# Performance work log

Measured on AMD Instinct MI355X. Metric: run time of the kernel, lower is better.

The kernel has to match this reference:

```python
import jax, jax.numpy as jnp
import numpy as np

HIDDEN = 1024
NUM_EXPERTS = 16
TOP_K = 6
EPS = 1e-10


def setup_inputs() -> dict:
    key = jax.random.key(0)
    k1, k2, k3, k4 = jax.random.split(key, 4)
    tokens = jax.random.normal(k1, (4, 2048, HIDDEN), dtype=jnp.float32)
    # torch.nn.Linear(hidden_size, num_experts): weight [E, H], bias [E]
    bound = 1.0 / np.sqrt(HIDDEN)
    router_w = jax.random.uniform(k2, (NUM_EXPERTS, HIDDEN), jnp.float32, -bound, bound)
    router_b = jax.random.uniform(k3, (NUM_EXPERTS,), jnp.float32, -bound, bound)
    # expert_weights = randn(E, H, H) / sqrt(H)
    expert_w = jax.random.normal(k4, (NUM_EXPERTS, HIDDEN, HIDDEN), dtype=jnp.float32) / np.sqrt(HIDDEN)
    return {"tokens": tokens, "router_w": router_w, "router_b": router_b, "expert_w": expert_w}


def reference(tokens, router_w, router_b, expert_w):
    B, S, H = tokens.shape
    E = expert_w.shape[0]
    T = B * S

    # Router: softmax -> top-k -> renormalize top-k probs
    logits = jnp.einsum("bsh,eh->bse", tokens, router_w) + router_b  # [B,S,E]
    probs = jax.nn.softmax(logits, axis=-1)
    top_p, top_i = jax.lax.top_k(probs, TOP_K)                        # [B,S,K]
    top_p = top_p / (jnp.sum(top_p, axis=-1, keepdims=True) + EPS)

    x = tokens.reshape(T, H)
    flat_i = top_i.reshape(T, TOP_K)
    flat_p = top_p.reshape(T, TOP_K)

    # Dense gate matrix [T, E]: scatter of normalized top-k weights.
    # Equivalent to the expand/sort/pad + weighted scatter-add restore.
    gate = jnp.zeros((T, E), dtype=flat_p.dtype)
    gate = gate.at[jnp.arange(T)[:, None], flat_i].add(flat_p)
    acc = jnp.maximum(jnp.sum(gate, axis=-1), EPS)  # weight accumulator (clamp min=1e-10)

    # Grouped GEMM equivalent: per-expert matmul weighted by gate, accumulated.
    out = jnp.zeros_like(x)
    for e in range(E):  # fixed, small structural loop over experts
        out = out + (x @ expert_w[e]) * gate[:, e:e + 1]
    out = (out / acc[:, None]).reshape(B, S, H)

    # 'dummy' gradient-connection term from restore_output_with_triton_and_gradients
    out = out + EPS * jnp.sum(top_p, axis=-1, keepdims=True)
    return out
```

## Files before the change

### kernel.cpp

```cpp
#include <hip/hip_runtime.h>
#include <cstdint>
#include <cstddef>

#define NE 16
#define TOPK 6
#define HID 1024
#define NTOK 8192
#define EPSF 1e-10f
#define CAP_ROWS 51200
#define MAXBLK 400

typedef short bf16x8 __attribute__((ext_vector_type(8)));
typedef float f32x4 __attribute__((ext_vector_type(4)));

__device__ __forceinline__ unsigned int f2bf_rne(float f) {
  union { float f; unsigned int u; } v;
  v.f = f;
  return (v.u + 0x7FFFu + ((v.u >> 16) & 1u)) >> 16;
}

__device__ __forceinline__ float bfbits2f(unsigned int hi16) {
  union { unsigned int u; float f; } v;
  v.u = hi16 << 16;
  return v.f;
}

__device__ __forceinline__ void load_lds16(const void* g, void* l) {
  __builtin_amdgcn_global_load_lds(
      (const __attribute__((address_space(1))) void*)g,
      (__attribute__((address_space(3))) void*)l, 16, 0, 0);
}

__global__ __launch_bounds__(256) void router_sparse_kernel(
    const float* __restrict__ tokens, const float* __restrict__ rw,
    const float* __restrict__ rb, unsigned short* __restrict__ Xb,
    unsigned int* __restrict__ topk, float* __restrict__ g6,
    float* __restrict__ epst) {
  __shared__ float s_rw[NE * HID];
  const int tid = threadIdx.x;
  const int wv = tid >> 6;
  const int lane = tid & 63;
  const int token = blockIdx.x * 4 + wv;

  for (int i = tid; i < NE * HID / 4; i += 256)
    ((float4*)s_rw)[i] = ((const float4*)rw)[i];
  __syncthreads();

  const float* xp = tokens + (size_t)token * HID;
  float x[16];
#pragma unroll
  for (int j = 0; j < 16; ++j) x[j] = xp[lane + 64 * j];

  unsigned short* xbrow = Xb + (size_t)token * HID;
#pragma unroll
  for (int j = 0; j < 16; ++j)
    xbrow[lane + 64 * j] = (unsigned short)f2bf_rne(x[j]);

  float lg[NE];
#pragma unroll
  for (int e = 0; e < NE; ++e) {
    const float* w = s_rw + e * HID;
    float p = 0.f;
#pragma unroll
    for (int j = 0; j < 16; ++j) p += x[j] * w[lane + 64 * j];
    lg[e] = p;
  }
#pragma unroll
  for (int m = 1; m < 64; m <<= 1) {
#pragma unroll
    for (int e = 0; e < NE; ++e) lg[e] += __shfl_xor(lg[e], m);
  }
  float mx = -1e30f;
#pragma unroll
  for (int e = 0; e < NE; ++e) {
    lg[e] += rb[e];
    mx = fmaxf(mx, lg[e]);
  }
  float q[NE];
  float s_all = 0.f;
#pragma unroll
  for (int e = 0; e < NE; ++e) {
    q[e] = expf(lg[e] - mx);
    s_all += q[e];
  }
  unsigned sel = 0, pack = 0;
  float s_top = 0.f;
  float gq[TOPK];
#pragma unroll
  for (int k = 0; k < TOPK; ++k) {
    float best = -1.f;
    int bi = 0;
#pragma unroll
    for (int e = 0; e < NE; ++e) {
      bool taken = (sel >> e) & 1u;
      if (!taken && q[e] > best) { best = q[e]; bi = e; }
    }
    sel |= 1u << bi;
    gq[k] = best;
    s_top += best;
    pack |= ((unsigned)bi) << (4 * k);
  }
  if (lane < TOPK)
    g6[(size_t)token * TOPK + lane] = gq[lane] / s_top;
  if (lane == 32) {
    topk[token] = pack;
    float s = s_top / s_all;
    epst[token] = EPSF * (s / (s + EPSF));
  }
}

__global__ __launch_bounds__(256) void sortassign_kernel(
    const unsigned int* __restrict__ topk, const float* __restrict__ g6,
    unsigned int* __restrict__ tokmap, float* __restrict__ gpos,
    unsigned int* __restrict__ inv, unsigned int* __restrict__ table,
    unsigned int* __restrict__ total) {
  __shared__ unsigned int hist[NE];
  __shared__ unsigned int s_seg[NE];
  __shared__ unsigned int s_sc[256];
  const int e = blockIdx.x;
  const int tid = threadIdx.x;

  if (tid < NE) hist[tid] = 0;
  __syncthreads();
  for (int t = tid; t < NTOK; t += 256) {
    const unsigned p = topk[t];
#pragma unroll
    for (int k = 0; k < TOPK; ++k) atomicAdd(&hist[(p >> (4 * k)) & 15u], 1u);
  }
  __syncthreads();
  if (tid == 0) {
    unsigned off = 0;
    for (int i = 0; i < NE; ++i) {
      s_seg[i] = off;
      off += ((hist[i] + 127) >> 7) << 7;
    }
  }
  __syncthreads();
  if (e == 0 && tid == 0) {
    unsigned b = 0;
    for (int i = 0; i < NE; ++i) {
      unsigned mb = (hist[i] + 127) >> 7;
      for (unsigned m = 0; m < mb; ++m)
        table[b++] = ((unsigned)i << 24) | (s_seg[i] + m * 128);
    }
    *total = b;
  }

  const int tbase = tid * (NTOK / 256);
  unsigned c = 0;
  for (int i = 0; i < NTOK / 256; ++i) {
    const unsigned p = topk[tbase + i];
#pragma unroll
    for (int k = 0; k < TOPK; ++k) c += (((p >> (4 * k)) & 15u) == (unsigned)e);
  }
  s_sc[tid] = c;
  __syncthreads();
  for (int off = 1; off < 256; off <<= 1) {
    unsigned v = (tid >= off) ? s_sc[tid - off] : 0u;
    __syncthreads();
    s_sc[tid] += v;
    __syncthreads();
  }
  const unsigned seg0 = s_seg[e];
  unsigned pos = seg0 + s_sc[tid] - c;
  for (int i = 0; i < NTOK / 256; ++i) {
    const int t = tbase + i;
    const unsigned p = topk[t];
#pragma unroll
    for (int k = 0; k < TOPK; ++k) {
      if (((p >> (4 * k)) & 15u) == (unsigned)e) {
        tokmap[pos] = (unsigned)t;
        gpos[pos] = g6[(size_t)t * TOPK + k];
        inv[(size_t)t * TOPK + k] = pos;
        ++pos;
      }
    }
  }
  const unsigned cnt_e = s_sc[255];
  const unsigned segend = seg0 + (((cnt_e + 127) >> 7) << 7);
  for (unsigned p2 = seg0 + cnt_e + tid; p2 < segend; p2 += 256) {
    tokmap[p2] = 0u;
    gpos[p2] = 0.f;
  }
}

__global__ __launch_bounds__(256) void cvt_wt_kernel(
    const float* __restrict__ w, unsigned short* __restrict__ wt) {
  __shared__ float tile[64][65];
  const int kt = blockIdx.x * 64;
  const int nt = blockIdx.y * 64;
  const int e = blockIdx.z;
  const int tr = threadIdx.x >> 6;
  const int tc = threadIdx.x & 63;
  const float* wp = w + (size_t)e * HID * HID;
#pragma unroll
  for (int r = 0; r < 64; r += 4)
    tile[r + tr][tc] = wp[(size_t)(kt + r + tr) * HID + nt + tc];
  __syncthreads();
  unsigned short* wo = wt + (size_t)e * HID * HID;
  const int a = threadIdx.x & 31;
  const int rg = threadIdx.x >> 5;
#pragma unroll
  for (int c = 0; c < 64; c += 8) {
    const int n = c + rg;
    const unsigned lo = f2bf_rne(tile[2 * a][n]);
    const unsigned hi = f2bf_rne(tile[2 * a + 1][n]);
    *(unsigned int*)(wo + (size_t)(nt + n) * HID + kt + 2 * a) = lo | (hi << 16);
  }
}

__global__ __launch_bounds__(256, 4) void moe_ggemm_kernel(
    const unsigned short* __restrict__ Xb, const unsigned short* __restrict__ Wt,
    const unsigned int* __restrict__ table, const unsigned int* __restrict__ total,
    const unsigned int* __restrict__ tokmap, const float* __restrict__ gpos,
    unsigned short* __restrict__ Y) {
  __shared__ unsigned short As[128 * 32];
  __shared__ unsigned short Bs[128 * 32];
  __shared__ unsigned int Ts[128];
  __shared__ float Gs[128];

  const unsigned tot = *total;
  const unsigned bx = blockIdx.x;
  const unsigned slot = bx >> 3;
  if (slot >= tot) return;
  const int n0 = (bx & 7) * 128;
  const unsigned ent = table[slot];
  const int e = ent >> 24;
  const int row0 = ent & 0xFFFFFF;

  const int tid = threadIdx.x;
  const int wv = tid >> 6;
  const int lane = tid & 63;
  const int lm = lane & 15;
  const int quad = lane >> 4;
  const int woff_m = (wv & 1) * 64;
  const int woff_n = (wv >> 1) * 64;

  if (tid < 128) {
    Ts[tid] = tokmap[row0 + tid];
    Gs[tid] = gpos[row0 + tid];
  }
  __syncthreads();

  const int srow = wv * 32 + (lane >> 2);
  const int schunk = (lane & 3) * 16;
  const char* gA0 = (const char*)Xb + (size_t)Ts[srow] * (HID * 2) + schunk;
  const char* gA1 = (const char*)Xb + (size_t)Ts[srow + 16] * (HID * 2) + schunk;
  const char* gB0 = (const char*)Wt + (size_t)e * (HID * HID * 2) +
                    (size_t)(n0 + srow) * (HID * 2) + schunk;
  const char* gB1 = gB0 + 16 * HID * 2;
  char* const lA0 = (char*)As + (wv * 32) * 64;
  char* const lA1 = lA0 + 16 * 64;
  char* const lB0 = (char*)Bs + (wv * 32) * 64;
  char* const lB1 = lB0 + 16 * 64;

  f32x4 acc[4][4];
#pragma unroll
  for (int i = 0; i < 4; ++i)
#pragma unroll
    for (int j = 0; j < 4; ++j) acc[i][j] = (f32x4){0.f, 0.f, 0.f, 0.f};

  for (int ks = 0; ks < 32; ++ks) {
    __syncthreads();
    load_lds16(gA0, lA0);
    load_lds16(gA1, lA1);
    load_lds16(gB0, lB0);
    load_lds16(gB1, lB1);
    gA0 += 64; gA1 += 64; gB0 += 64; gB1 += 64;
    __syncthreads();

    bf16x8 a[4], b[4];
#pragma unroll
    for (int i = 0; i < 4; ++i)
      a[i] = *(const bf16x8*)((const char*)As +
                              (woff_m + 16 * i + lm) * 64 + quad * 16);
#pragma unroll
    for (int j = 0; j < 4; ++j)
      b[j] = *(const bf16x8*)((const char*)Bs +
                              (woff_n + 16 * j + lm) * 64 + quad * 16);
#pragma unroll
    for (int i = 0; i < 4; ++i)
#pragma unroll
      for (int j = 0; j < 4; ++j)
        acc[i][j] =
            __builtin_amdgcn_mfma_f32_16x16x32_bf16(a[i], b[j], acc[i][j], 0, 0, 0);
  }

#pragma unroll
  for (int i = 0; i < 4; ++i)
#pragma unroll
    for (int r = 0; r < 4; ++r) {
      const int row = woff_m + 16 * i + quad * 4 + r;
      const float g = Gs[row];
      unsigned short* yrow = Y + (size_t)(row0 + row) * HID + n0;
#pragma unroll
      for (int j = 0; j < 4; ++j)
        yrow[woff_n + 16 * j + lm] = (unsigned short)f2bf_rne(g * acc[i][j][r]);
    }
}

__global__ __launch_bounds__(256) void reduce_kernel(
    const unsigned short* __restrict__ Y, const unsigned int* __restrict__ inv,
    const float* __restrict__ epst, float* __restrict__ out) {
  const int sub = threadIdx.x >> 7;
  const int ct = threadIdx.x & 127;
  const int t = blockIdx.x * 2 + sub;
  const int c0 = ct * 8;

  float s[8];
  const float ep = epst[t];
#pragma unroll
  for (int i = 0; i < 8; ++i) s[i] = ep;

#pragma unroll
  for (int k = 0; k < TOPK; ++k) {
    const unsigned pos = inv[(size_t)t * TOPK + k];
    const uint4 v = *(const uint4*)(Y + (size_t)pos * HID + c0);
    s[0] += bfbits2f(v.x & 0xFFFFu);
    s[1] += bfbits2f(v.x >> 16);
    s[2] += bfbits2f(v.y & 0xFFFFu);
    s[3] += bfbits2f(v.y >> 16);
    s[4] += bfbits2f(v.z & 0xFFFFu);
    s[5] += bfbits2f(v.z >> 16);
    s[6] += bfbits2f(v.w & 0xFFFFu);
    s[7] += bfbits2f(v.w >> 16);
  }
  float* orow = out + (size_t)t * HID + c0;
  *(float4*)orow = (float4){s[0], s[1], s[2], s[3]};
  *(float4*)(orow + 4) = (float4){s[4], s[5], s[6], s[7]};
}

extern "C" void kernel_launch(void* const* d_in, const int* in_sizes, int n_in,
                              void* d_out, int out_size, void* d_ws, size_t ws_size,
                              hipStream_t stream) {
  const float* tokens = (const float*)d_in[0];
  const float* rw = (const float*)d_in[1];
  const float* rb = (const float*)d_in[2];
  const float* ew = (const float*)d_in[3];
  float* out = (float*)d_out;

  char* ws = (char*)d_ws;
  const size_t OFF_XB = 0;
  const size_t OFF_WT = 16777216;
  const size_t OFF_Y = 50331648;
  const size_t OFF_META = 155189248;
  const size_t M_TOKMAP = OFF_META + 0;
  const size_t M_GPOS = OFF_META + 204800;
  const size_t M_TOTAL = OFF_META + 409600;
  const size_t M_TABLE = OFF_META + 409664;
  const size_t M_INV = OFF_META + 411328;
  const size_t M_TOPK = OFF_META + 607936;
  const size_t M_G6 = OFF_META + 640704;
  const size_t M_EPST = OFF_META + 837312;

  unsigned short* Xb = (unsigned short*)(ws + OFF_XB);
  unsigned short* Wt = (unsigned short*)(ws + OFF_WT);
  unsigned short* Y = (unsigned short*)(ws + OFF_Y);
  unsigned int* tokmap = (unsigned int*)(ws + M_TOKMAP);
  float* gpos = (float*)(ws + M_GPOS);
  unsigned int* total = (unsigned int*)(ws + M_TOTAL);
  unsigned int* table = (unsigned int*)(ws + M_TABLE);
  unsigned int* inv = (unsigned int*)(ws + M_INV);
  unsigned int* topk = (unsigned int*)(ws + M_TOPK);
  float* g6 = (float*)(ws + M_G6);
  float* epst = (float*)(ws + M_EPST);

  router_sparse_kernel<<<dim3(NTOK / 4), dim3(256), 0, stream>>>(
      tokens, rw, rb, Xb, topk, g6, epst);
  cvt_wt_kernel<<<dim3(HID / 64, HID / 64, NE), dim3(256), 0, stream>>>(ew, Wt);
  sortassign_kernel<<<dim3(NE), dim3(256), 0, stream>>>(
      topk, g6, tokmap, gpos, inv, table, total);
  moe_ggemm_kernel<<<dim3(MAXBLK * 8), dim3(256), 0, stream>>>(
      Xb, Wt, table, total, tokmap, gpos, Y);
  reduce_kernel<<<dim3(NTOK / 2), dim3(256), 0, stream>>>(Y, inv, epst, out);
}
```

Before: 399.0 us.

## Widen GEMM K-step, batch router tokens per block, pack histogram counters

The grouped GEMM now loads two 32-wide K slices per barrier pair into doubled LDS buffers, halving the number of synchronisations per tile. The router processes four tokens per wave with float4 loads and packed bf16 stores, so the 64KB router weight copy into LDS is amortised over more tokens. The sort/assign kernel counts expert hits in packed 8-bit register counters, replacing per-element LDS atomics, and reuses those counts for the prefix scan. Risks include higher LDS use, which lowers GEMM occupancy, and fewer router blocks. The packed counters also assume no expert exceeds 255 hits per thread, which holds with 32 tokens per thread.

```diff
diff --git a/kernel.cpp b/kernel.cpp
--- a/kernel.cpp
+++ b/kernel.cpp
@@ -40,72 +40,83 @@
   const int tid = threadIdx.x;
   const int wv = tid >> 6;
   const int lane = tid & 63;
-  const int token = blockIdx.x * 4 + wv;
 
   for (int i = tid; i < NE * HID / 4; i += 256)
     ((float4*)s_rw)[i] = ((const float4*)rw)[i];
   __syncthreads();
 
-  const float* xp = tokens + (size_t)token * HID;
-  float x[16];
-#pragma unroll
-  for (int j = 0; j < 16; ++j) x[j] = xp[lane + 64 * j];
-
-  unsigned short* xbrow = Xb + (size_t)token * HID;
-#pragma unroll
-  for (int j = 0; j < 16; ++j)
-    xbrow[lane + 64 * j] = (unsigned short)f2bf_rne(x[j]);
-
-  float lg[NE];
-#pragma unroll
-  for (int e = 0; e < NE; ++e) {
-    const float* w = s_rw + e * HID;
-    float p = 0.f;
-#pragma unroll
-    for (int j = 0; j < 16; ++j) p += x[j] * w[lane + 64 * j];
-    lg[e] = p;
-  }
-#pragma unroll
-  for (int m = 1; m < 64; m <<= 1) {
-#pragma unroll
-    for (int e = 0; e < NE; ++e) lg[e] += __shfl_xor(lg[e], m);
-  }
-  float mx = -1e30f;
-#pragma unroll
-  for (int e = 0; e < NE; ++e) {
-    lg[e] += rb[e];
-    mx = fmaxf(mx, lg[e]);
-  }
-  float q[NE];
-  float s_all = 0.f;
-#pragma unroll
-  for (int e = 0; e < NE; ++e) {
-    q[e] = expf(lg[e] - mx);
-    s_all += q[e];
-  }
-  unsigned sel = 0, pack = 0;
-  float s_top = 0.f;
-  float gq[TOPK];
-#pragma unroll
-  for (int k = 0; k < TOPK; ++k) {
-    float best = -1.f;
-    int bi = 0;
+  for (int ti = 0; ti < 4; ++ti) {
+    const int token = blockIdx.x * 16 + wv * 4 + ti;
+    const float* xp = tokens + (size_t)token * HID;
+
+    float4 x4[4];
+#pragma unroll
+    for (int c = 0; c < 4; ++c)
+      x4[c] = *(const float4*)(xp + lane * 4 + 256 * c);
+
+    unsigned short* xbrow = Xb + (size_t)token * HID;
+#pragma unroll
+    for (int c = 0; c < 4; ++c) {
+      uint2 o;
+      o.x = f2bf_rne(x4[c].x) | (f2bf_rne(x4[c].y) << 16);
+      o.y = f2bf_rne(x4[c].z) | (f2bf_rne(x4[c].w) << 16);
+      *(uint2*)(xbrow + lane * 4 + 256 * c) = o;
+    }
+
+    float lg[NE];
 #pragma unroll
     for (int e = 0; e < NE; ++e) {
-      bool taken = (sel >> e) & 1u;
-      if (!taken && q[e] > best) { best = q[e]; bi = e; }
-    }
-    sel |= 1u << bi;
-    gq[k] = best;
-    s_top += best;
-    pack |= ((unsigned)bi) << (4 * k);
-  }
-  if (lane < TOPK)
-    g6[(size_t)token * TOPK + lane] = gq[lane] / s_top;
-  if (lane == 32) {
-    topk[token] = pack;
-    float s = s_top / s_all;
-    epst[token] = EPSF * (s / (s + EPSF));
+      const float4* w4 = (const float4*)(s_rw + e * HID);
+      float p = 0.f;
+#pragma unroll
+      for (int c = 0; c < 4; ++c) {
+        const float4 w = w4[lane + 64 * c];
+        p += x4[c].x * w.x + x4[c].y * w.y + x4[c].z * w.z + x4[c].w * w.w;
+      }
+      lg[e] = p;
+    }
+#pragma unroll
+    for (int m = 1; m < 64; m <<= 1) {
+#pragma unroll
+      for (int e = 0; e < NE; ++e) lg[e] += __shfl_xor(lg[e], m);
+    }
+    float mx = -1e30f;
+#pragma unroll
+    for (int e = 0; e < NE; ++e) {
+      lg[e] += rb[e];
+      mx = fmaxf(mx, lg[e]);
+    }
+    float q[NE];
+    float s_all = 0.f;
+#pragma unroll
+    for (int e = 0; e < NE; ++e) {
+      q[e] = expf(lg[e] - mx);
+      s_all += q[e];
+    }
+    unsigned sel = 0, pack = 0;
+    float s_top = 0.f;
+    float gq[TOPK];
+#pragma unroll
+    for (int k = 0; k < TOPK; ++k) {
+      float best = -1.f;
+      int bi = 0;
+#pragma unroll
+      for (int e = 0; e < NE; ++e) {
+        bool taken = (sel >> e) & 1u;
+        if (!taken && q[e] > best) { best = q[e]; bi = e; }
+      }
+      sel |= 1u << bi;
+      gq[k] = best;
+      s_top += best;
+      pack |= ((unsigned)bi) << (4 * k);
+    }
+    if (lane < TOPK)
+      g6[(size_t)token * TOPK + lane] = gq[lane] / s_top;
+    if (lane == 32) {
+      topk[token] = pack;
+      float s = s_top / s_all;
+      epst[token] = EPSF * (s / (s + EPSF));
+    }
   }
 }
 
@@ -122,10 +133,23 @@
 
   if (tid < NE) hist[tid] = 0;
   __syncthreads();
-  for (int t = tid; t < NTOK; t += 256) {
-    const unsigned p = topk[t];
-#pragma unroll
-    for (int k = 0; k < TOPK; ++k) atomicAdd(&hist[(p >> (4 * k)) & 15u], 1u);
+
+  unsigned long long clo = 0ull, chi = 0ull;
+  for (int i = 0; i < NTOK / 256; ++i) {
+    const unsigned p = topk[i * 256 + tid];
+#pragma unroll
+    for (int k = 0; k < TOPK; ++k) {
+      const unsigned nib = (p >> (4 * k)) & 15u;
+      if (nib < 8) clo += 1ull << (8 * nib);
+      else chi += 1ull << (8 * (nib - 8));
+    }
+  }
+#pragma unroll
+  for (int j = 0; j < 8; ++j) {
+    unsigned v = (unsigned)((clo >> (8 * j)) & 255u);
+    if (v) atomicAdd(&hist[j], v);
+    v = (unsigned)((chi >> (8 * j)) & 255u);
+    if (v) atomicAdd(&hist[8 + j], v);
   }
   __syncthreads();
   if (tid == 0) {
@@ -146,13 +170,8 @@
     *total = b;
   }
 
-  const int tbase = tid * (NTOK / 256);
-  unsigned c = 0;
-  for (int i = 0; i < NTOK / 256; ++i) {
-    const unsigned p = topk[tbase + i];
-#pragma unroll
-    for (int k = 0; k < TOPK; ++k) c += (((p >> (4 * k)) & 15u) == (unsigned)e);
-  }
+  const unsigned c =
+      (unsigned)(((e < 8 ? (clo >> (8 * e)) : (chi >> (8 * (e - 8))))) & 255u);
   s_sc[tid] = c;
   __syncthreads();
   for (int off = 1; off < 256; off <<= 1) {
@@ -164,7 +183,7 @@
   const unsigned seg0 = s_seg[e];
   unsigned pos = seg0 + s_sc[tid] - c;
   for (int i = 0; i < NTOK / 256; ++i) {
-    const int t = tbase + i;
+    const int t = i * 256 + tid;
     const unsigned p = topk[t];
 #pragma unroll
     for (int k = 0; k < TOPK; ++k) {
@@ -214,8 +233,8 @@
     const unsigned int* __restrict__ table, const unsigned int* __restrict__ total,
     const unsigned int* __restrict__ tokmap, const float* __restrict__ gpos,
     unsigned short* __restrict__ Y) {
-  __shared__ unsigned short As[128 * 32];
-  __shared__ unsigned short Bs[128 * 32];
+  __shared__ unsigned short As[2][128 * 32];
+  __shared__ unsigned short Bs[2][128 * 32];
   __shared__ unsigned int Ts[128];
   __shared__ float Gs[128];
 
@@ -253,6 +272,7 @@
   char* const lA1 = lA0 + 16 * 64;
   char* const lB0 = (char*)Bs + (wv * 32) * 64;
   char* const lB1 = lB0 + 16 * 64;
+  const int HB = 128 * 32 * 2;
 
   f32x4 acc[4][4];
 #pragma unroll
@@ -260,30 +280,37 @@
 #pragma unroll
     for (int j = 0; j < 4; ++j) acc[i][j] = (f32x4){0.f, 0.f, 0.f, 0.f};
 
-  for (int ks = 0; ks < 32; ++ks) {
+  for (int ks = 0; ks < 16; ++ks) {
     __syncthreads();
     load_lds16(gA0, lA0);
     load_lds16(gA1, lA1);
+    load_lds16(gA0 + 64, lA0 + HB);
+    load_lds16(gA1 + 64, lA1 + HB);
     load_lds16(gB0, lB0);
     load_lds16(gB1, lB1);
-    gA0 += 64; gA1 += 64; gB0 += 64; gB1 += 64;
+    load_lds16(gB0 + 64, lB0 + HB);
+    load_lds16(gB1 + 64, lB1 + HB);
+    gA0 += 128; gA1 += 128; gB0 += 128; gB1 += 128;
     __syncthreads();
 
-    bf16x8 a[4], b[4];
-#pragma unroll
-    for (int i = 0; i < 4; ++i)
-      a[i] = *(const bf16x8*)((const char*)As +
-                              (woff_m + 16 * i + lm) * 64 + quad * 16);
-#pragma unroll
-    for (int j = 0; j < 4; ++j)
-      b[j] = *(const bf16x8*)((const char*)Bs +
-                              (woff_n + 16 * j + lm) * 64 + quad * 16);
-#pragma unroll
-    for (int i = 0; i < 4; ++i)
+#pragma unroll
+    for (int kh = 0; kh < 2; ++kh) {
+      bf16x8 a[4], b[4];
+#pragma unroll
+      for (int i = 0; i < 4; ++i)
+        a[i] = *(const bf16x8*)((const char*)As + kh * HB +
+                                (woff_m + 16 * i + lm) * 64 + quad * 16);
 #pragma unroll
       for (int j = 0; j < 4; ++j)
-        acc[i][j] =
-            __builtin_amdgcn_mfma_f32_16x16x32_bf16(a[i], b[j], acc[i][j], 0, 0, 0);
+        b[j] = *(const bf16x8*)((const char*)Bs + kh * HB +
+                                (woff_n + 16 * j + lm) * 64 + quad * 16);
+#pragma unroll
+      for (int i = 0; i < 4; ++i)
+#pragma unroll
+        for (int j = 0; j < 4; ++j)
+          acc[i][j] =
+              __builtin_amdgcn_mfma_f32_16x16x32_bf16(a[i], b[j], acc[i][j], 0, 0, 0);
+    }
   }
 
 #pragma unroll
@@ -365,7 +392,7 @@
   float* g6 = (float*)(ws + M_G6);
   float* epst = (float*)(ws + M_EPST);
 
-  router_sparse_kernel<<<dim3(NTOK / 4), dim3(256), 0, stream>>>(
+  router_sparse_kernel<<<dim3(NTOK / 16), dim3(256), 0, stream>>>(
       tokens, rw, rb, Xb, topk, g6, epst);
   cvt_wt_kernel<<<dim3(HID / 64, HID / 64, NE), dim3(256), 0, stream>>>(ew, Wt);
   sortassign_kernel<<<dim3(NE), dim3(256), 0, stream>>>(
```

Result: slower. 452.0 us (+13.3%).
